# Performance work log

Hardware: AMD Instinct MI355X
Metric: run time of the kernel (lower is better)

The kernel has to match this reference:

```python
import jax, jax.numpy as jnp
import numpy as np

# Dims: batch N, time T, joints V=9, K=5 adjacency partitions (spatial strategy, max_hop=2),
# in channels 16, out channels = coords = 3, temporal kernel 9 (ConvTranspose, stride 1, pad 4).
N, T, V, C_IN, C_OUT, K, KT = 256, 2048, 9, 16, 3, 5, 9


def setup_inputs() -> dict:
    key = jax.random.key(0)
    ks = jax.random.split(key, 6)
    pose_feats = jax.random.normal(ks[0], (N, T, V * C_IN), jnp.float32)
    # Fixed (non-trainable) multi-partition normalized adjacency A2: [K, V, V].
    # Graph values come from ted_db constants in the repo; stand-in: row-normalized random.
    A = jax.random.uniform(ks[1], (K, V, V), jnp.float32)
    A = A / jnp.sum(A, axis=-1, keepdims=True)
    # GCN 1x1 conv: in -> K*C_OUT channels
    W_gcn = jax.random.normal(ks[2], (K, C_OUT, C_IN), jnp.float32) * (1.0 / np.sqrt(C_IN))
    b_gcn = jax.random.normal(ks[3], (K, C_OUT), jnp.float32) * 0.02
    # Temporal ConvTranspose2d(C_OUT, C_OUT, kernel=(9,1), stride=(1,1), padding=(4,0));
    # torch weight layout [in, out, kH, kW]
    W_tcn = jax.random.normal(ks[4], (C_OUT, C_OUT, KT, 1), jnp.float32) * (1.0 / np.sqrt(C_OUT * KT))
    b_tcn = jax.random.normal(ks[5], (C_OUT,), jnp.float32) * 0.02
    return {"pose_feats": pose_feats, "A": A, "W_gcn": W_gcn, "b_gcn": b_gcn,
            "W_tcn": W_tcn, "b_tcn": b_tcn}


def _st_gcn_transpose(x, A, W_gcn, b_gcn, W_tcn, b_tcn):
    # x: [n, c_in, t, v]
    # 1x1 conv to K*C_OUT channels, then adjacency contraction over partitions k
    y = jnp.einsum('nctv,koc->nkotv', x, W_gcn) + b_gcn[None, :, :, None, None]
    y = jnp.einsum('nkotv,kvw->notw', y, A)  # [n, c_out, t, v]
    # temporal transposed conv, kernel (9,1), stride 1, torch padding 4 -> jax pad (4,4)
    y = jax.lax.conv_transpose(y, W_tcn, strides=(1, 1), padding=[(4, 4), (0, 0)],
                               dimension_numbers=('NCHW', 'IOHW', 'NCHW'),
                               transpose_kernel=True)
    y = y + b_tcn[None, :, None, None]
    return jax.nn.leaky_relu(y, 0.01)


def reference(pose_feats, A, W_gcn, b_gcn, W_tcn, b_tcn):
    n, t, f = pose_feats.shape
    x = pose_feats.reshape(n, t, V, C_IN).transpose(0, 3, 1, 2)  # [n, c_in, t, v]
    y = _st_gcn_transpose(x, A, W_gcn, b_gcn, W_tcn, b_tcn)      # [n, c_out, t, v]
    return y.transpose(0, 2, 3, 1).reshape(n, t, V * C_OUT)       # [n, t, 27]
```

## Files before the change

kernel.cpp:

```cpp
#include <hip/hip_runtime.h>

typedef short short8 __attribute__((ext_vector_type(8)));
typedef float f32x4  __attribute__((ext_vector_type(4)));

constexpr int N_    = 256;
constexpr int T_    = 2048;
constexpr int V_    = 9;
constexpr int FIN_  = 144;
constexpr int J_    = 27;
constexpr int KT_   = 9;
constexpr int THREADS_ = 128;
constexpr int TILE_ = 120;
constexpr int NTILE_ = 18;
constexpr int ZROWS_ = 128;
constexpr int ZS_ = 28;

constexpr int BF_OFF_F = 0;
constexpr int B0_OFF   = 2560;
constexpr int WT_OFF   = 2587;
constexpr int BT_OFF   = 2668;

__device__ __forceinline__ unsigned short bf16_rne(float x) {
    unsigned u = __float_as_uint(x);
    u = (u + 0x7FFFu + ((u >> 16) & 1u)) >> 16;
    return (unsigned short)u;
}
__device__ __forceinline__ unsigned pk2(float a, float b) {
    return (unsigned)bf16_rne(a) | ((unsigned)bf16_rne(b) << 16);
}

__global__ void setup_weights(const float* __restrict__ A,
                              const float* __restrict__ Wg,
                              const float* __restrict__ bg,
                              const float* __restrict__ Wt_in,
                              const float* __restrict__ bt,
                              float* __restrict__ ws) {
    __shared__ float Wc[FIN_ * J_];
    const int tid = threadIdx.x;
    for (int idx = tid; idx < FIN_ * J_; idx += 256) {
        const int f = idx / J_, j = idx % J_;
        const int v = f >> 4, c = f & 15;
        const int w = j / 3, o = j % 3;
        float s = 0.f;
        #pragma unroll
        for (int k = 0; k < 5; ++k)
            s += Wg[(k * 3 + o) * 16 + c] * A[(k * 9 + v) * 9 + w];
        Wc[idx] = s;
    }
    __syncthreads();
    unsigned short* bfp = (unsigned short*)(ws + BF_OFF_F);
    for (int i = tid; i < 5120; i += 256) {
        const int e = i & 7, lane = (i >> 3) & 63, nt = (i >> 9) & 1, s = i >> 10;
        const int k = s * 32 + (lane >> 4) * 8 + e;
        const int n = nt * 16 + (lane & 15);
        const float val = (k < FIN_ && n < J_) ? Wc[k * J_ + n] : 0.f;
        bfp[i] = bf16_rne(val);
    }
    if (tid < J_) {
        const int w = tid / 3, o = tid % 3;
        float s = 0.f;
        #pragma unroll
        for (int k = 0; k < 5; ++k) {
            float cs = 0.f;
            #pragma unroll
            for (int v = 0; v < V_; ++v) cs += A[(k * 9 + v) * 9 + w];
            s += bg[k * 3 + o] * cs;
        }
        ws[B0_OFF + tid] = s;
    }
    if (tid < 81) {
        const int o = tid / 27, r = tid % 27, o2 = r / 9, dd = r % 9;
        ws[WT_OFF + tid] = Wt_in[(o2 * 3 + o) * 9 + (8 - dd)];
    }
    if (tid < 3) ws[BT_OFF + tid] = bt[tid];
}

__global__ __launch_bounds__(THREADS_, 3) void fused_stgcn(const float* __restrict__ pose,
                                                           const float* __restrict__ cw,
                                                           float* __restrict__ out) {
    __shared__ __align__(16) float zbuf[ZROWS_ * ZS_];

    const int tid  = threadIdx.x;
    const int bid  = blockIdx.x;
    const int nb   = bid / NTILE_;
    const int tile = bid % NTILE_;
    const int t0   = tile * TILE_;
    const int lane = tid & 63;
    const int wv   = tid >> 6;
    const int g8   = lane >> 4;
    const int j0   = lane & 15;

    short8 bfrag[5][2];
    {
        const short8* bsrc = (const short8*)(cw + BF_OFF_F);
        #pragma unroll
        for (int s = 0; s < 5; ++s)
            #pragma unroll
            for (int nt = 0; nt < 2; ++nt)
                bfrag[s][nt] = bsrc[(s * 2 + nt) * 64 + lane];
    }
    const float b0n0 = cw[B0_OFF + j0];
    const float b0n1 = (j0 < 11) ? cw[B0_OFF + 16 + j0] : 0.f;

    const size_t nrow0 = (size_t)nb * T_;

    auto issue = [&](int mt, float4* Av, float4* Bv) {
        const int text = t0 - 4 + wv * 64 + mt * 16 + j0;
        const bool okr = (text >= 0 && text < T_);
        const float* rowp = pose + (nrow0 + (okr ? text : 0)) * FIN_;
        #pragma unroll
        for (int s = 0; s < 5; ++s) {
            const int k0 = s * 32 + g8 * 8;
            const bool ok = okr && (k0 < FIN_);
            Av[s] = ok ? *(const float4*)(rowp + k0)     : make_float4(0.f, 0.f, 0.f, 0.f);
            Bv[s] = ok ? *(const float4*)(rowp + k0 + 4) : make_float4(0.f, 0.f, 0.f, 0.f);
        }
    };
    auto process = [&](int mt, const float4* Av, const float4* Bv) {
        short8 af[5];
        #pragma unroll
        for (int s = 0; s < 5; ++s) {
            union { unsigned u[4]; short8 s8; } cvu;
            cvu.u[0] = pk2(Av[s].x, Av[s].y);
            cvu.u[1] = pk2(Av[s].z, Av[s].w);
            cvu.u[2] = pk2(Bv[s].x, Bv[s].y);
            cvu.u[3] = pk2(Bv[s].z, Bv[s].w);
            af[s] = cvu.s8;
        }
        f32x4 acc0 = {0.f, 0.f, 0.f, 0.f};
        f32x4 acc1 = {0.f, 0.f, 0.f, 0.f};
        #pragma unroll
        for (int s = 0; s < 5; ++s) {
            acc0 = __builtin_amdgcn_mfma_f32_16x16x32_bf16(af[s], bfrag[s][0], acc0, 0, 0, 0);
            acc1 = __builtin_amdgcn_mfma_f32_16x16x32_bf16(af[s], bfrag[s][1], acc1, 0, 0, 0);
        }
        #pragma unroll
        for (int r = 0; r < 4; ++r) {
            const int zrow = wv * 64 + mt * 16 + g8 * 4 + r;
            const int text = t0 - 4 + zrow;
            const bool okz = (text >= 0 && text < T_);
            zbuf[zrow * ZS_ + j0] = okz ? acc0[r] + b0n0 : 0.f;
            if (j0 < 11)
                zbuf[zrow * ZS_ + 16 + j0] = okz ? acc1[r] + b0n1 : 0.f;
        }
    };

    float4 A0[5], B0v[5], A1[5], B1[5];
    issue(0, A0, B0v);
    issue(1, A1, B1);
    process(0, A0, B0v);
    issue(2, A0, B0v);
    process(1, A1, B1);
    issue(3, A1, B1);
    process(2, A0, B0v);
    process(3, A1, B1);
    __syncthreads();

    const int rows_out = min(TILE_, T_ - t0);
    float oacc[J_];
    if (tid < rows_out) {
        #pragma unroll
        for (int w = 0; w < V_; ++w)
            #pragma unroll
            for (int o2 = 0; o2 < 3; ++o2)
                oacc[w * 3 + o2] = cw[BT_OFF + o2];
        #pragma unroll
        for (int dd = 0; dd < KT_; ++dd) {
            union { f32x4 v4[7]; float f[28]; } zu;
            const f32x4* zp = (const f32x4*)&zbuf[(tid + dd) * ZS_];
            #pragma unroll
            for (int c = 0; c < 7; ++c) zu.v4[c] = zp[c];
            #pragma unroll
            for (int o = 0; o < 3; ++o) {
                #pragma unroll
                for (int o2 = 0; o2 < 3; ++o2) {
                    const float wt = cw[WT_OFF + o * 27 + o2 * 9 + dd];
                    #pragma unroll
                    for (int w = 0; w < V_; ++w)
                        oacc[w * 3 + o2] = fmaf(zu.f[w * 3 + o], wt, oacc[w * 3 + o2]);
                }
            }
        }
        #pragma unroll
        for (int j = 0; j < J_; ++j) oacc[j] = fmaxf(oacc[j], 0.01f * oacc[j]);
    }
    __syncthreads();
    if (tid < rows_out) {
        #pragma unroll
        for (int j = 0; j < J_; ++j) zbuf[tid * J_ + j] = oacc[j];
    }
    __syncthreads();

    const int total4 = (rows_out * J_) / 4;
    float4* dst4 = (float4*)(out + (nrow0 + t0) * J_);
    const float4* src4 = (const float4*)zbuf;
    for (int idx = tid; idx < total4; idx += THREADS_)
        dst4[idx] = src4[idx];
}

extern "C" void kernel_launch(void* const* d_in, const int* in_sizes, int n_in,
                              void* d_out, int out_size, void* d_ws, size_t ws_size,
                              hipStream_t stream) {
    const float* pose = (const float*)d_in[0];
    const float* A    = (const float*)d_in[1];
    const float* Wg   = (const float*)d_in[2];
    const float* bg   = (const float*)d_in[3];
    const float* Wt   = (const float*)d_in[4];
    const float* bt   = (const float*)d_in[5];
    float* ws   = (float*)d_ws;
    float* outp = (float*)d_out;

    setup_weights<<<1, 256, 0, stream>>>(A, Wg, bg, Wt, bt, ws);
    fused_stgcn<<<N_ * NTILE_, THREADS_, 0, stream>>>(pose, ws, outp);
}
```

Before: 87.11 us.

## Process three time tiles per block with cross-tile prefetch of input rows

Each block now loops over three consecutive time tiles instead of one. It issues the global loads for the next tile's first two row groups while the current tile's MFMA, temporal conv and store phases run. The block count drops threefold, the launch-bounds occupancy hint falls from 3 to 2, and __syncthreads is replaced with an explicit lgkmcnt wait plus barrier. This amortises the per-block weight-fragment loads and hides load latency behind compute, at the cost of fewer blocks in flight and a serial dependency chain inside each block.

New measurement: 100.9 us. 15.9% more time.

```diff
diff --git a/kernel.cpp b/kernel.cpp
--- a/kernel.cpp
+++ b/kernel.cpp
@@ -10,10 +10,12 @@
 constexpr int J_    = 27;
 constexpr int KT_   = 9;
 constexpr int THREADS_ = 128;
-constexpr int TILE_ = 120;
+constexpr int TILE_  = 120;
 constexpr int NTILE_ = 18;
+constexpr int CHUNK_ = 3;
+constexpr int BLKPN_ = NTILE_ / CHUNK_;
 constexpr int ZROWS_ = 128;
-constexpr int ZS_ = 28;
+constexpr int ZS_    = 28;
 
 constexpr int BF_OFF_F = 0;
 constexpr int B0_OFF   = 2560;
@@ -75,20 +77,25 @@
     if (tid < 3) ws[BT_OFF + tid] = bt[tid];
 }
 
-__global__ __launch_bounds__(THREADS_, 3) void fused_stgcn(const float* __restrict__ pose,
+__global__ __launch_bounds__(THREADS_, 2) void fused_stgcn(const float* __restrict__ pose,
                                                            const float* __restrict__ cw,
                                                            float* __restrict__ out) {
     __shared__ __align__(16) float zbuf[ZROWS_ * ZS_];
 
     const int tid  = threadIdx.x;
     const int bid  = blockIdx.x;
-    const int nb   = bid / NTILE_;
-    const int tile = bid % NTILE_;
-    const int t0   = tile * TILE_;
+    const int nb   = bid / BLKPN_;
+    const int c0   = (bid % BLKPN_) * CHUNK_;
     const int lane = tid & 63;
     const int wv   = tid >> 6;
     const int g8   = lane >> 4;
     const int j0   = lane & 15;
+    const size_t nrow0 = (size_t)nb * T_;
+
+    auto WB = []() {
+        asm volatile("s_waitcnt lgkmcnt(0)" ::: "memory");
+        __builtin_amdgcn_s_barrier();
+    };
 
     short8 bfrag[5][2];
     {
@@ -102,9 +109,7 @@
     const float b0n0 = cw[B0_OFF + j0];
     const float b0n1 = (j0 < 11) ? cw[B0_OFF + 16 + j0] : 0.f;
 
-    const size_t nrow0 = (size_t)nb * T_;
-
-    auto issue = [&](int mt, float4* Av, float4* Bv) {
+    auto issue = [&](int t0, int mt, float4* Av, float4* Bv) {
         const int text = t0 - 4 + wv * 64 + mt * 16 + j0;
         const bool okr = (text >= 0 && text < T_);
         const float* rowp = pose + (nrow0 + (okr ? text : 0)) * FIN_;
@@ -116,7 +121,7 @@
             Bv[s] = ok ? *(const float4*)(rowp + k0 + 4) : make_float4(0.f, 0.f, 0.f, 0.f);
         }
     };
-    auto process = [&](int mt, const float4* Av, const float4* Bv) {
+    auto process = [&](int t0, int mt, const float4* Av, const float4* Bv) {
         short8 af[5];
         #pragma unroll
         for (int s = 0; s < 5; ++s) {
@@ -145,57 +150,66 @@
         }
     };
 
-    float4 A0[5], B0v[5], A1[5], B1[5];
-    issue(0, A0, B0v);
-    issue(1, A1, B1);
-    process(0, A0, B0v);
-    issue(2, A0, B0v);
-    process(1, A1, B1);
-    issue(3, A1, B1);
-    process(2, A0, B0v);
-    process(3, A1, B1);
-    __syncthreads();
-
-    const int rows_out = min(TILE_, T_ - t0);
-    float oacc[J_];
-    if (tid < rows_out) {
-        #pragma unroll
-        for (int w = 0; w < V_; ++w)
-            #pragma unroll
-            for (int o2 = 0; o2 < 3; ++o2)
-                oacc[w * 3 + o2] = cw[BT_OFF + o2];
-        #pragma unroll
-        for (int dd = 0; dd < KT_; ++dd) {
-            union { f32x4 v4[7]; float f[28]; } zu;
-            const f32x4* zp = (const f32x4*)&zbuf[(tid + dd) * ZS_];
-            #pragma unroll
-            for (int c = 0; c < 7; ++c) zu.v4[c] = zp[c];
-            #pragma unroll
-            for (int o = 0; o < 3; ++o) {
+    float4 A0v[5], B0v[5], A1v[5], B1v[5];
+    int t0 = c0 * TILE_;
+    issue(t0, 0, A0v, B0v);
+    issue(t0, 1, A1v, B1v);
+
+    #pragma unroll 1
+    for (int i = 0; i < CHUNK_; ++i) {
+        const int t0n = t0 + TILE_;
+        const bool more = (i + 1 < CHUNK_);
+
+        process(t0, 0, A0v, B0v);  issue(t0, 2, A0v, B0v);
+        process(t0, 1, A1v, B1v);  issue(t0, 3, A1v, B1v);
+        process(t0, 2, A0v, B0v);  if (more) issue(t0n, 0, A0v, B0v);
+        process(t0, 3, A1v, B1v);  if (more) issue(t0n, 1, A1v, B1v);
+        WB();
+
+        const int rows_out = min(TILE_, T_ - t0);
+        float oacc[J_];
+        if (tid < rows_out) {
+            #pragma unroll
+            for (int w = 0; w < V_; ++w)
                 #pragma unroll
-                for (int o2 = 0; o2 < 3; ++o2) {
-                    const float wt = cw[WT_OFF + o * 27 + o2 * 9 + dd];
+                for (int o2 = 0; o2 < 3; ++o2)
+                    oacc[w * 3 + o2] = cw[BT_OFF + o2];
+            #pragma unroll
+            for (int dd = 0; dd < KT_; ++dd) {
+                union { f32x4 v4[7]; float f[28]; } zu;
+                const f32x4* zp = (const f32x4*)&zbuf[(tid + dd) * ZS_];
+                #pragma unroll
+                for (int c = 0; c < 7; ++c) zu.v4[c] = zp[c];
+                #pragma unroll
+                for (int o = 0; o < 3; ++o) {
                     #pragma unroll
-                    for (int w = 0; w < V_; ++w)
-                        oacc[w * 3 + o2] = fmaf(zu.f[w * 3 + o], wt, oacc[w * 3 + o2]);
+                    for (int o2 = 0; o2 < 3; ++o2) {
+                        const float wt = cw[WT_OFF + o * 27 + o2 * 9 + dd];
+                        #pragma unroll
+                        for (int w = 0; w < V_; ++w)
+                            oacc[w * 3 + o2] = fmaf(zu.f[w * 3 + o], wt, oacc[w * 3 + o2]);
+                    }
                 }
             }
-        }
-        #pragma unroll
-        for (int j = 0; j < J_; ++j) oacc[j] = fmaxf(oacc[j], 0.01f * oacc[j]);
-    }
-    __syncthreads();
-    if (tid < rows_out) {
-        #pragma unroll
-        for (int j = 0; j < J_; ++j) zbuf[tid * J_ + j] = oacc[j];
-    }
-    __syncthreads();
-
-    const int total4 = (rows_out * J_) / 4;
-    float4* dst4 = (float4*)(out + (nrow0 + t0) * J_);
-    const float4* src4 = (const float4*)zbuf;
-    for (int idx = tid; idx < total4; idx += THREADS_)
-        dst4[idx] = src4[idx];
+            #pragma unroll
+            for (int j = 0; j < J_; ++j) oacc[j] = fmaxf(oacc[j], 0.01f * oacc[j]);
+        }
+        WB();
+        if (tid < rows_out) {
+            #pragma unroll
+            for (int j = 0; j < J_; ++j) zbuf[tid * J_ + j] = oacc[j];
+        }
+        WB();
+
+        const int total4 = (rows_out * J_) / 4;
+        float4* dst4 = (float4*)(out + (nrow0 + t0) * J_);
+        const float4* src4 = (const float4*)zbuf;
+        for (int idx = tid; idx < total4; idx += THREADS_)
+            dst4[idx] = src4[idx];
+        WB();
+
+        t0 = t0n;
+    }
 }
 
 extern "C" void kernel_launch(void* const* d_in, const int* in_sizes, int n_in,
@@ -211,5 +225,5 @@
     float* outp = (float*)d_out;
 
     setup_weights<<<1, 256, 0, stream>>>(A, Wg, bg, Wt, bt, ws);
-    fused_stgcn<<<N_ * NTILE_, THREADS_, 0, stream>>>(pose, ws, outp);
-}
+    fused_stgcn<<<N_ * BLKPN_, THREADS_, 0, stream>>>(pose, ws, outp);
+}
```

## Split fused kernel into GEMM pass and temporal-conv pass via bf16 intermediate

Applied to the files above, without the earlier changes.

Splits the single fused kernel into two kernels. The first is a grid-strided MFMA GEMM with no halo overlap that writes the graph-conv result as bf16 to workspace. The second reloads that result with a halo and runs the 9-tap temporal transposed conv, bias and leaky-relu. This removes the redundant halo GEMM rows (128 computed per 120 output rows) and the per-tile boundary predication. In exchange it adds a round trip of roughly 28 MB through global memory, an extra launch, and an extra bf16 rounding of the intermediate.

Result: slower. 109.2 us (+25.3%).

```diff
diff --git a/kernel.cpp b/kernel.cpp
--- a/kernel.cpp
+++ b/kernel.cpp
@@ -9,16 +9,16 @@
 constexpr int FIN_  = 144;
 constexpr int J_    = 27;
 constexpr int KT_   = 9;
-constexpr int THREADS_ = 128;
-constexpr int TILE_ = 120;
-constexpr int NTILE_ = 18;
-constexpr int ZROWS_ = 128;
-constexpr int ZS_ = 28;
-
-constexpr int BF_OFF_F = 0;
-constexpr int B0_OFF   = 2560;
-constexpr int WT_OFF   = 2587;
-constexpr int BT_OFF   = 2668;
+constexpr int ZPS_  = 28;
+constexpr int TT_   = N_ * T_ / 16;
+constexpr int K1B_  = 1024;
+constexpr int K1W_  = K1B_ * 4;
+constexpr int TILE2_ = 248;
+constexpr int NT2_   = 9;
+
+constexpr int BF_OFF_F  = 0;
+constexpr int B0_OFF    = 2560;
+constexpr int ZWS_OFF_F = 4096;
 
 __device__ __forceinline__ unsigned short bf16_rne(float x) {
     unsigned u = __float_as_uint(x);
@@ -28,12 +28,12 @@
 __device__ __forceinline__ unsigned pk2(float a, float b) {
     return (unsigned)bf16_rne(a) | ((unsigned)bf16_rne(b) << 16);
 }
+__device__ __forceinline__ float bflo(unsigned u) { return __uint_as_float(u << 16); }
+__device__ __forceinline__ float bfhi(unsigned u) { return __uint_as_float(u & 0xFFFF0000u); }
 
 __global__ void setup_weights(const float* __restrict__ A,
                               const float* __restrict__ Wg,
                               const float* __restrict__ bg,
-                              const float* __restrict__ Wt_in,
-                              const float* __restrict__ bt,
                               float* __restrict__ ws) {
     __shared__ float Wc[FIN_ * J_];
     const int tid = threadIdx.x;
@@ -68,27 +68,17 @@
         }
         ws[B0_OFF + tid] = s;
     }
-    if (tid < 81) {
-        const int o = tid / 27, r = tid % 27, o2 = r / 9, dd = r % 9;
-        ws[WT_OFF + tid] = Wt_in[(o2 * 3 + o) * 9 + (8 - dd)];
-    }
-    if (tid < 3) ws[BT_OFF + tid] = bt[tid];
-}
-
-__global__ __launch_bounds__(THREADS_, 3) void fused_stgcn(const float* __restrict__ pose,
-                                                           const float* __restrict__ cw,
-                                                           float* __restrict__ out) {
-    __shared__ __align__(16) float zbuf[ZROWS_ * ZS_];
-
+}
+
+__global__ __launch_bounds__(256) void k1_gemm(const float* __restrict__ pose,
+                                               const float* __restrict__ cw,
+                                               unsigned short* __restrict__ zg) {
     const int tid  = threadIdx.x;
-    const int bid  = blockIdx.x;
-    const int nb   = bid / NTILE_;
-    const int tile = bid % NTILE_;
-    const int t0   = tile * TILE_;
     const int lane = tid & 63;
     const int wv   = tid >> 6;
     const int g8   = lane >> 4;
     const int j0   = lane & 15;
+    const int wgid = blockIdx.x * 4 + wv;
 
     short8 bfrag[5][2];
     {
@@ -102,21 +92,19 @@
     const float b0n0 = cw[B0_OFF + j0];
     const float b0n1 = (j0 < 11) ? cw[B0_OFF + 16 + j0] : 0.f;
 
-    const size_t nrow0 = (size_t)nb * T_;
-
-    auto issue = [&](int mt, float4* Av, float4* Bv) {
-        const int text = t0 - 4 + wv * 64 + mt * 16 + j0;
-        const bool okr = (text >= 0 && text < T_);
-        const float* rowp = pose + (nrow0 + (okr ? text : 0)) * FIN_;
+    auto issue = [&](int t16, float4* Av, float4* Bv) {
+        const int nb = t16 >> 7;
+        const int tr = (t16 & 127) << 4;
+        const float* rowp = pose + ((size_t)nb * T_ + tr + j0) * FIN_;
         #pragma unroll
         for (int s = 0; s < 5; ++s) {
-            const int k0 = s * 32 + g8 * 8;
-            const bool ok = okr && (k0 < FIN_);
-            Av[s] = ok ? *(const float4*)(rowp + k0)     : make_float4(0.f, 0.f, 0.f, 0.f);
-            Bv[s] = ok ? *(const float4*)(rowp + k0 + 4) : make_float4(0.f, 0.f, 0.f, 0.f);
+            int k0 = s * 32 + g8 * 8;
+            if (k0 > 136) k0 = 128;
+            Av[s] = *(const float4*)(rowp + k0);
+            Bv[s] = *(const float4*)(rowp + k0 + 4);
         }
     };
-    auto process = [&](int mt, const float4* Av, const float4* Bv) {
+    auto process = [&](int t16, const float4* Av, const float4* Bv) {
         short8 af[5];
         #pragma unroll
         for (int s = 0; s < 5; ++s) {
@@ -134,47 +122,75 @@
             acc0 = __builtin_amdgcn_mfma_f32_16x16x32_bf16(af[s], bfrag[s][0], acc0, 0, 0, 0);
             acc1 = __builtin_amdgcn_mfma_f32_16x16x32_bf16(af[s], bfrag[s][1], acc1, 0, 0, 0);
         }
+        const int nb = t16 >> 7;
+        const int tr = (t16 & 127) << 4;
+        unsigned short* zr = zg + ((size_t)nb * T_ + tr) * ZPS_;
         #pragma unroll
         for (int r = 0; r < 4; ++r) {
-            const int zrow = wv * 64 + mt * 16 + g8 * 4 + r;
-            const int text = t0 - 4 + zrow;
-            const bool okz = (text >= 0 && text < T_);
-            zbuf[zrow * ZS_ + j0] = okz ? acc0[r] + b0n0 : 0.f;
-            if (j0 < 11)
-                zbuf[zrow * ZS_ + 16 + j0] = okz ? acc1[r] + b0n1 : 0.f;
+            unsigned short* p = zr + (g8 * 4 + r) * ZPS_;
+            p[j0] = bf16_rne(acc0[r] + b0n0);
+            if (j0 < 11) p[16 + j0] = bf16_rne(acc1[r] + b0n1);
         }
     };
 
-    float4 A0[5], B0v[5], A1[5], B1[5];
-    issue(0, A0, B0v);
-    issue(1, A1, B1);
-    process(0, A0, B0v);
-    issue(2, A0, B0v);
-    process(1, A1, B1);
-    issue(3, A1, B1);
-    process(2, A0, B0v);
-    process(3, A1, B1);
-    __syncthreads();
-
-    const int rows_out = min(TILE_, T_ - t0);
+    float4 Aa[5], Ba[5], Ab[5], Bb[5];
+    issue(wgid, Aa, Ba);
+    #pragma unroll 1
+    for (int i = 0; i < 8; i += 2) {
+        const int t = wgid + i * K1W_;
+        issue(t + K1W_, Ab, Bb);
+        process(t, Aa, Ba);
+        if (i < 6) issue(t + 2 * K1W_, Aa, Ba);
+        process(t + K1W_, Ab, Bb);
+    }
+}
+
+__global__ __launch_bounds__(256) void k2_tcn(const unsigned short* __restrict__ zg,
+                                              const float* __restrict__ Wt_in,
+                                              const float* __restrict__ bt,
+                                              float* __restrict__ out) {
+    __shared__ __align__(16) float zb[256 * ZPS_];
+
+    const int tid  = threadIdx.x;
+    const int bid  = blockIdx.x;
+    const int nb   = bid / NT2_;
+    const int tile = bid % NT2_;
+    const int t0   = tile * TILE2_;
+
+    const unsigned* zg32 = (const unsigned*)zg;
+    #pragma unroll
+    for (int q = 0; q < 14; ++q) {
+        const int d  = q * 256 + tid;
+        const int rl = d / 14, c2 = d % 14;
+        const int row = t0 - 4 + rl;
+        const bool ok = (row >= 0 && row < T_);
+        const unsigned u = ok ? zg32[((size_t)nb * T_ + row) * (ZPS_ / 2) + c2] : 0u;
+        float2 f;
+        f.x = bflo(u);
+        f.y = bfhi(u);
+        *(float2*)&zb[2 * d] = f;
+    }
+    __syncthreads();
+
+    const int rows_out = min(TILE2_, T_ - t0);
     float oacc[J_];
     if (tid < rows_out) {
         #pragma unroll
         for (int w = 0; w < V_; ++w)
             #pragma unroll
             for (int o2 = 0; o2 < 3; ++o2)
-                oacc[w * 3 + o2] = cw[BT_OFF + o2];
+                oacc[w * 3 + o2] = bt[o2];
         #pragma unroll
         for (int dd = 0; dd < KT_; ++dd) {
             union { f32x4 v4[7]; float f[28]; } zu;
-            const f32x4* zp = (const f32x4*)&zbuf[(tid + dd) * ZS_];
+            const f32x4* zp = (const f32x4*)&zb[(tid + dd) * ZPS_];
             #pragma unroll
             for (int c = 0; c < 7; ++c) zu.v4[c] = zp[c];
             #pragma unroll
             for (int o = 0; o < 3; ++o) {
                 #pragma unroll
                 for (int o2 = 0; o2 < 3; ++o2) {
-                    const float wt = cw[WT_OFF + o * 27 + o2 * 9 + dd];
+                    const float wt = Wt_in[(o2 * 3 + o) * KT_ + (KT_ - 1 - dd)];
                     #pragma unroll
                     for (int w = 0; w < V_; ++w)
                         oacc[w * 3 + o2] = fmaf(zu.f[w * 3 + o], wt, oacc[w * 3 + o2]);
@@ -187,14 +203,14 @@
     __syncthreads();
     if (tid < rows_out) {
         #pragma unroll
-        for (int j = 0; j < J_; ++j) zbuf[tid * J_ + j] = oacc[j];
+        for (int j = 0; j < J_; ++j) zb[tid * J_ + j] = oacc[j];
     }
     __syncthreads();
 
     const int total4 = (rows_out * J_) / 4;
-    float4* dst4 = (float4*)(out + (nrow0 + t0) * J_);
-    const float4* src4 = (const float4*)zbuf;
-    for (int idx = tid; idx < total4; idx += THREADS_)
+    float4* dst4 = (float4*)(out + ((size_t)nb * T_ + t0) * J_);
+    const float4* src4 = (const float4*)zb;
+    for (int idx = tid; idx < total4; idx += 256)
         dst4[idx] = src4[idx];
 }
 
@@ -208,8 +224,10 @@
     const float* Wt   = (const float*)d_in[4];
     const float* bt   = (const float*)d_in[5];
     float* ws   = (float*)d_ws;
+    unsigned short* zg = (unsigned short*)(ws + ZWS_OFF_F);
     float* outp = (float*)d_out;
 
-    setup_weights<<<1, 256, 0, stream>>>(A, Wg, bg, Wt, bt, ws);
-    fused_stgcn<<<N_ * NTILE_, THREADS_, 0, stream>>>(pose, ws, outp);
-}
+    setup_weights<<<1, 256, 0, stream>>>(A, Wg, bg, ws);
+    k1_gemm<<<K1B_, 256, 0, stream>>>(pose, ws, zg);
+    k2_tcn<<<N_ * NT2_, 256, 0, stream>>>(zg, Wt, bt, outp);
+}
```
